# Kernel optimization log

Hardware: AMD Instinct MI355X
Metric: run time of the kernel (lower is better)

The kernel has to match this reference:

```python
import jax, jax.numpy as jnp
import numpy as np

NEG_INF = -1e30
EPS = 1e-7  # keras.backend.epsilon()


def _ctc_loss(y_true, y_pred):
    """Faithful CTC loss matching keras ctc_batch_cost + tf v1 ctc_loss.

    y_true: [B, L] int labels (no blanks), all rows full length L.
    y_pred: [B, T, C] probabilities; tf ctc_loss re-softmaxes log(p+eps).
    Blank index = C - 1. Returns loss [B, 1].
    """
    B, T, C = y_pred.shape
    L = y_true.shape[1]
    S = 2 * L + 1
    blank = C - 1

    # keras passes log(y_pred+eps) as logits; tf ctc_loss applies softmax
    lp = jax.nn.log_softmax(jnp.log(y_pred + EPS), axis=-1)  # [B,T,C]

    # extended label sequence: blank, l0, blank, l1, ..., blank  [B,S]
    ext = jnp.full((B, S), blank, dtype=y_true.dtype)
    ext = ext.at[:, 1::2].set(y_true)

    # skip transition (s-2 -> s) allowed iff ext[s] != blank and ext[s] != ext[s-2]
    same_as_2back = jnp.concatenate(
        [jnp.ones((B, 2), bool), ext[:, 2:] == ext[:, :-2]], axis=1)
    can_skip = (ext != blank) & (~same_as_2back)  # [B,S]

    # emission log-prob of each lattice state at each time: [B,T,S]
    lp_ext = jnp.take_along_axis(lp, ext[:, None, :], axis=2)

    # alpha init at t=0: only states 0 (blank) and 1 (first label) reachable
    alpha0 = jnp.full((B, S), NEG_INF, dtype=lp.dtype)
    alpha0 = alpha0.at[:, 0].set(lp_ext[:, 0, 0])
    alpha0 = alpha0.at[:, 1].set(lp_ext[:, 0, 1])

    pad1 = jnp.full((B, 1), NEG_INF, dtype=lp.dtype)
    pad2 = jnp.full((B, 2), NEG_INF, dtype=lp.dtype)

    def step(alpha, lp_t):
        a_stay = alpha
        a_prev = jnp.concatenate([pad1, alpha[:, :-1]], axis=1)
        a_skip = jnp.where(can_skip,
                           jnp.concatenate([pad2, alpha[:, :-2]], axis=1),
                           NEG_INF)
        m = jnp.maximum(a_stay, jnp.maximum(a_prev, a_skip))
        lse = m + jnp.log(jnp.exp(a_stay - m) + jnp.exp(a_prev - m)
                          + jnp.exp(a_skip - m))
        return lse + lp_t, None

    # scan over remaining T-1 time steps
    alphaT, _ = jax.lax.scan(step, alpha0, jnp.swapaxes(lp_ext, 0, 1)[1:])

    # total log-likelihood: end at last blank or last label
    loglik = jnp.logaddexp(alphaT[:, S - 1], alphaT[:, S - 2])
    return -loglik[:, None]  # [B,1], matches expand_dims(..., 1)


def setup_inputs() -> dict:
    key = jax.random.key(0)
    k1, k2 = jax.random.split(key)
    B, T, C, L = 128, 1024, 128, 128
    y_true = jax.random.randint(k1, (B, L), 0, C - 1, dtype=jnp.int32)
    y_pred = jax.random.uniform(k2, (B, T, C), dtype=jnp.float32)
    return {"y_true": y_true, "y_pred": y_pred}


def reference(y_true, y_pred):
    return _ctc_loss(y_true, y_pred)
```

## Files before the change

### kernel.cpp

```cpp
#include <hip/hip_runtime.h>

#define TT 1024
#define CC 128
#define LL 128
#define EPSF 1e-7f
#define LN2F 0.69314718055994531f

#define LOG2F(x) __builtin_amdgcn_logf(x)

typedef unsigned int uint;

template <int CTRL>
__device__ __forceinline__ int dpp_i(int old_, int x) {
  return __builtin_amdgcn_update_dpp(old_, x, CTRL, 0xf, 0xf, false);
}
template <int CTRL>
__device__ __forceinline__ float dpp0f(float x) {
  return __uint_as_float((uint)__builtin_amdgcn_update_dpp(
      0, (int)__float_as_uint(x), CTRL, 0xf, 0xf, true));
}
__device__ __forceinline__ float dpp_shr1_f32(float x) {
  return __uint_as_float((uint)__builtin_amdgcn_update_dpp(
      0, (int)__float_as_uint(x), 0x138, 0xf, 0xf, true));
}
__device__ __forceinline__ float readlane63_f(float v) {
  return __uint_as_float(
      (uint)__builtin_amdgcn_readlane((int)__float_as_uint(v), 63));
}

__device__ __forceinline__ uint bf16bits(float x) {
  uint u = __float_as_uint(x);
  return (u + 0x7fffu + ((u >> 16) & 1u)) >> 16;
}

__device__ __forceinline__ float bperm(int byteaddr, float v) {
  return __uint_as_float(
      (uint)__builtin_amdgcn_ds_bpermute(byteaddr, (int)__float_as_uint(v)));
}


#define CTC_STEP(wv, pbf)                                   \
  do {                                                      \
    const float p1 = __uint_as_float((wv) << 16);           \
    const float p2 = __uint_as_float((wv) & 0xffff0000u);   \
    const float pb = (pbf);                                 \
    const float p3 = dpp_shr1_f32(a3);                      \
    const float n0 = (a0 + p3) * pb;                        \
    const float n1 = __builtin_fmaf(s1f, p3, a0 + a1) * p1; \
    const float n2 = (a2 + a1) * pb;                        \
    const float n3 = __builtin_fmaf(s3f, a1, a3 + a2) * p2; \
    const float n4 = (a4 + a3) * pb;                        \
    a0 = n0; a1 = n1; a2 = n2; a3 = n3; a4 = n4;            \
  } while (0)

#define CTC_QUAD(et, eb)      \
  do {                        \
    CTC_STEP((et).x, (eb).x); \
    CTC_STEP((et).y, (eb).y); \
    CTC_STEP((et).z, (eb).z); \
    CTC_STEP((et).w, (eb).w); \
  } while (0)

#define CTC_RESCALE()                                                \
  do {                                                               \
    const float m = fmaxf(fmaxf(fmaxf(a0, a1), fmaxf(a2, a3)), a4);  \
    int ke = (int)(__float_as_uint(m) >> 23);                        \
    ke = max(ke, dpp_i<0x111>(ke, ke));                              \
    ke = max(ke, dpp_i<0x112>(ke, ke));                              \
    ke = max(ke, dpp_i<0x114>(ke, ke));                              \
    ke = max(ke, dpp_i<0x118>(ke, ke));                              \
    ke = max(ke, dpp_i<0x142>(ke, ke));                              \
    ke = max(ke, dpp_i<0x143>(ke, ke));                              \
    ke = __builtin_amdgcn_readlane(ke, 63);                          \
    int e = ke - 227;             \
    e = e < -127 ? -127 : e;                                         \
    const float sc = __uint_as_float((uint)(127 - e) << 23);         \
    a0 *= sc; a1 *= sc; a2 *= sc; a3 *= sc; a4 *= sc;                \
    ell += e;                                                        \
  } while (0)

#define STAGE8(t0)                                                          \
  do {                                                                      \
    float2 vv[8];                                                           \
    _Pragma("unroll") for (int j = 0; j < 8; ++j)                           \
        vv[j] = *(const float2*)(Pb + (size_t)((t0) + j) * CC);             \
    float ss[8];                                                            \
    _Pragma("unroll") for (int j = 0; j < 8; ++j)                           \
        ss[j] = (vv[j].x + vv[j].y) + (2.0f * EPSF);                        \
    _Pragma("unroll") for (int j = 0; j < 8; ++j)                           \
        ss[j] += dpp0f<0x111>(ss[j]);                        \
    _Pragma("unroll") for (int j = 0; j < 8; ++j)                           \
        ss[j] += dpp0f<0x112>(ss[j]);                        \
    _Pragma("unroll") for (int j = 0; j < 8; ++j)                           \
        ss[j] += dpp0f<0x114>(ss[j]);                        \
    _Pragma("unroll") for (int j = 0; j < 8; ++j)                           \
        ss[j] += dpp0f<0x118>(ss[j]);                        \
    _Pragma("unroll") for (int j = 0; j < 8; ++j)                           \
        ss[j] += dpp0f<0x142>(ss[j]);                      \
    _Pragma("unroll") for (int j = 0; j < 8; ++j)                           \
        ss[j] += dpp0f<0x143>(ss[j]);    \
    _Pragma("unroll") for (int q = 0; q < 2; ++q) {                         \
      uint wds[4];                                                          \
      float nys[4];                                                         \
      _Pragma("unroll") for (int c = 0; c < 4; ++c) {                       \
        const int j = q * 4 + c;                                            \
        const float x = readlane63_f(ss[j]);                                \
        const float r = 1.0f / x;                                           \
        const float er = EPSF * r;                                          \
        const float nx = __builtin_fmaf(vv[j].x, r, er);                    \
        const float ny = __builtin_fmaf(vv[j].y, r, er);                    \
        const float c1a = bperm(gxb, nx), c1b = bperm(gxb, ny);             \
        const float c2a = bperm(gyb, nx), c2b = bperm(gyb, ny);             \
        const float g1 = sx ? c1b : c1a;                                    \
        const float g2 = sy ? c2b : c2a;                                    \
        wds[c] = (bf16bits(g2) << 16) | bf16bits(g1);                       \
        nys[c] = ny;                                                        \
      }                                                                     \
      const int tq = (t0) + q * 4;                                          \
      uint4 val;                                                            \
      val.x = wds[0]; val.y = wds[1]; val.z = wds[2]; val.w = wds[3];       \
      *(uint4*)((char*)ETl + ((tq >> 5) & 3) * 8192 +                       \
                ((tq >> 2) & 7) * 1024 + L * 16) = val;                     \
      if (L == 63) {                                                        \
        float4 e4;                                                          \
        e4.x = nys[0]; e4.y = nys[1]; e4.z = nys[2]; e4.w = nys[3];         \
        *(float4*)&EBl[tq] = e4;                                            \
      }                                                                     \
    }                                                                       \
  } while (0)

__global__ __launch_bounds__(320) void ctc_fused(const int* __restrict__ yt,
                                                 const float* __restrict__ yp,
                                                 float* __restrict__ out) {
  const int b = blockIdx.x;
  const int tid = threadIdx.x;
  const int L = tid & 63;
  const int w = tid >> 6;

  __shared__ uint4 ETl[4][8][64];
  __shared__ __align__(16) float EBl[TT];

  const int2 lab = *(const int2*)(yt + b * LL + 2 * L);

  const int labm1 = __shfl_up(lab.y, 1);
  const float s1f = ((L > 0) && (lab.x != labm1)) ? 1.0f : 0.0f;
  const float s3f = (lab.y != lab.x) ? 1.0f : 0.0f;

  const float* Pb = yp + (size_t)b * TT * CC + 2 * L;
  const int gxb = (lab.x >> 1) << 2, gyb = (lab.y >> 1) << 2;
  const int sx = lab.x & 1, sy = lab.y & 1;

  if (w != 0) {
    STAGE8((w - 1) * 8);
    STAGE8(32 + (w - 1) * 8);
  }
  __syncthreads();

  uint4 etA = {0, 0, 0, 0}, etB = {0, 0, 0, 0};
  float4 ebA = {0, 0, 0, 0}, ebB = {0, 0, 0, 0};
  if (w == 0) {
    etA = ((const uint4*)ETl)[L];
    ebA = *(const float4*)&EBl[0];
  }

  float a0 = (w == 0 && L == 0) ? 0x1.0p100f : 0.0f;
  float a1 = 0.0f, a2 = 0.0f, a3 = 0.0f, a4 = 0.0f;
  int ell = -100;

#pragma unroll 1
  for (int kk = 0; kk < 32; ++kk) {
    if (w == 0) {
      const uint4* cur = (const uint4*)ETl + (size_t)(kk & 3) * 512;
      const float4* ebp = (const float4*)&EBl[kk * 32];
      etB = cur[1 * 64 + L]; ebB = ebp[1];
      CTC_QUAD(etA, ebA);
      etA = cur[2 * 64 + L]; ebA = ebp[2];
      CTC_QUAD(etB, ebB);
      etB = cur[3 * 64 + L]; ebB = ebp[3];
      CTC_QUAD(etA, ebA);
      etA = cur[4 * 64 + L]; ebA = ebp[4];
      CTC_QUAD(etB, ebB);
      CTC_RESCALE();
      etB = cur[5 * 64 + L]; ebB = ebp[5];
      CTC_QUAD(etA, ebA);
      etA = cur[6 * 64 + L]; ebA = ebp[6];
      CTC_QUAD(etB, ebB);
      etB = cur[7 * 64 + L]; ebB = ebp[7];
      CTC_QUAD(etA, ebA);
      etA = ((const uint4*)ETl)[(size_t)((kk + 1) & 3) * 512 + L];
      ebA = *(const float4*)&EBl[(kk < 31) ? (kk + 1) * 32 : 1020];
      CTC_QUAD(etB, ebB);
      CTC_RESCALE();
    } else if (kk < 30) {
      STAGE8((kk + 2) * 32 + (w - 1) * 8);
    }
    __syncthreads();
  }

  if (tid == 63) {
    float s = a3 + a4;
    if (s < 1e-37f) s = 1e-37f;
    out[b] = -LN2F * ((float)ell + LOG2F(s));
  }
}

extern "C" void kernel_launch(void* const* d_in, const int* in_sizes, int n_in,
                              void* d_out, int out_size, void* d_ws,
                              size_t ws_size, hipStream_t stream) {
  (void)d_ws; (void)ws_size; (void)n_in; (void)out_size;
  const int* yt = (const int*)d_in[0];
  const float* yp = (const float*)d_in[1];
  float* out = (float*)d_out;
  const int B = in_sizes[0] / LL;
  hipLaunchKernelGGL(ctc_fused, dim3(B), dim3(320), 0, stream, yt, yp, out);
}
```

Baseline: 144.1 us.

## Use three producer waves with packed bf16 bpermute gathers for emission staging

Cuts the block from five waves to four: three producer waves now stage 4-timestep groups in round-robin (8 groups per 32-step chunk) instead of four waves doing 8 steps each. Each gather now packs both normalized probabilities into one bf16 pair before a single ds_bpermute per label slot, halving the bpermute count, with the high or low half chosen afterward. This lowers wave count and LDS permute traffic per staged chunk. In exchange each producer wave does more work per chunk (two or three groups), which may lengthen the producer critical path relative to the single consumer wave.

```diff
diff --git a/kernel.cpp b/kernel.cpp
--- a/kernel.cpp
+++ b/kernel.cpp
@@ -31,11 +31,6 @@
 __device__ __forceinline__ uint bf16bits(float x) {
   uint u = __float_as_uint(x);
   return (u + 0x7fffu + ((u >> 16) & 1u)) >> 16;
-}
-
-__device__ __forceinline__ float bperm(int byteaddr, float v) {
-  return __uint_as_float(
-      (uint)__builtin_amdgcn_ds_bpermute(byteaddr, (int)__float_as_uint(v)));
 }
 
 
@@ -79,57 +74,64 @@
     ell += e;                                                        \
   } while (0)
 
-#define STAGE8(t0)                                                          \
+#define ST_LOAD(S, qg)                                          \
+  do {                                                          \
+    const float* Pq = Pb + (size_t)(qg) * 4 * CC + 2 * L;       \
+    vv##S##0 = *(const float2*)(Pq + 0 * CC);                   \
+    vv##S##1 = *(const float2*)(Pq + 1 * CC);                   \
+    vv##S##2 = *(const float2*)(Pq + 2 * CC);                   \
+    vv##S##3 = *(const float2*)(Pq + 3 * CC);                   \
+  } while (0)
+
+#define ST_COMP(S, qg)                                                      \
   do {                                                                      \
-    float2 vv[8];                                                           \
-    _Pragma("unroll") for (int j = 0; j < 8; ++j)                           \
-        vv[j] = *(const float2*)(Pb + (size_t)((t0) + j) * CC);             \
-    float ss[8];                                                            \
-    _Pragma("unroll") for (int j = 0; j < 8; ++j)                           \
-        ss[j] = (vv[j].x + vv[j].y) + (2.0f * EPSF);                        \
-    _Pragma("unroll") for (int j = 0; j < 8; ++j)                           \
+    const float2 vr0 = vv##S##0, vr1 = vv##S##1;                            \
+    const float2 vr2 = vv##S##2, vr3 = vv##S##3;                            \
+    const float2 vr[4] = {vr0, vr1, vr2, vr3};                              \
+    float ss[4];                                                            \
+    ss[0] = (vr0.x + vr0.y) + (2.0f * EPSF);                                \
+    ss[1] = (vr1.x + vr1.y) + (2.0f * EPSF);                                \
+    ss[2] = (vr2.x + vr2.y) + (2.0f * EPSF);                                \
+    ss[3] = (vr3.x + vr3.y) + (2.0f * EPSF);                                \
+    _Pragma("unroll") for (int j = 0; j < 4; ++j)                           \
         ss[j] += dpp0f<0x111>(ss[j]);                        \
-    _Pragma("unroll") for (int j = 0; j < 8; ++j)                           \
+    _Pragma("unroll") for (int j = 0; j < 4; ++j)                           \
         ss[j] += dpp0f<0x112>(ss[j]);                        \
-    _Pragma("unroll") for (int j = 0; j < 8; ++j)                           \
+    _Pragma("unroll") for (int j = 0; j < 4; ++j)                           \
         ss[j] += dpp0f<0x114>(ss[j]);                        \
-    _Pragma("unroll") for (int j = 0; j < 8; ++j)                           \
+    _Pragma("unroll") for (int j = 0; j < 4; ++j)                           \
         ss[j] += dpp0f<0x118>(ss[j]);                        \
-    _Pragma("unroll") for (int j = 0; j < 8; ++j)                           \
+    _Pragma("unroll") for (int j = 0; j < 4; ++j)                           \
         ss[j] += dpp0f<0x142>(ss[j]);                      \
-    _Pragma("unroll") for (int j = 0; j < 8; ++j)                           \
+    _Pragma("unroll") for (int j = 0; j < 4; ++j)                           \
         ss[j] += dpp0f<0x143>(ss[j]);    \
-    _Pragma("unroll") for (int q = 0; q < 2; ++q) {                         \
-      uint wds[4];                                                          \
-      float nys[4];                                                         \
-      _Pragma("unroll") for (int c = 0; c < 4; ++c) {                       \
-        const int j = q * 4 + c;                                            \
-        const float x = readlane63_f(ss[j]);                                \
-        const float r = 1.0f / x;                                           \
-        const float er = EPSF * r;                                          \
-        const float nx = __builtin_fmaf(vv[j].x, r, er);                    \
-        const float ny = __builtin_fmaf(vv[j].y, r, er);                    \
-        const float c1a = bperm(gxb, nx), c1b = bperm(gxb, ny);             \
-        const float c2a = bperm(gyb, nx), c2b = bperm(gyb, ny);             \
-        const float g1 = sx ? c1b : c1a;                                    \
-        const float g2 = sy ? c2b : c2a;                                    \
-        wds[c] = (bf16bits(g2) << 16) | bf16bits(g1);                       \
-        nys[c] = ny;                                                        \
-      }                                                                     \
-      const int tq = (t0) + q * 4;                                          \
-      uint4 val;                                                            \
-      val.x = wds[0]; val.y = wds[1]; val.z = wds[2]; val.w = wds[3];       \
-      *(uint4*)((char*)ETl + ((tq >> 5) & 3) * 8192 +                       \
-                ((tq >> 2) & 7) * 1024 + L * 16) = val;                     \
-      if (L == 63) {                                                        \
-        float4 e4;                                                          \
-        e4.x = nys[0]; e4.y = nys[1]; e4.z = nys[2]; e4.w = nys[3];         \
-        *(float4*)&EBl[tq] = e4;                                            \
-      }                                                                     \
+    uint wds[4];                                                            \
+    float nys[4];                                                           \
+    _Pragma("unroll") for (int j = 0; j < 4; ++j) {                         \
+      const float r = 1.0f / readlane63_f(ss[j]);                           \
+      const float er = EPSF * r;                                            \
+      const float nx = __builtin_fmaf(vr[j].x, r, er);                      \
+      const float ny = __builtin_fmaf(vr[j].y, r, er);                      \
+      const uint pk = (bf16bits(ny) << 16) | bf16bits(nx);                  \
+      const uint wx = (uint)__builtin_amdgcn_ds_bpermute(gxb, (int)pk);     \
+      const uint wy = (uint)__builtin_amdgcn_ds_bpermute(gyb, (int)pk);     \
+      const uint bx = sx ? (wx >> 16) : (wx & 0xffffu);                     \
+      const uint by = sy ? (wy >> 16) : (wy & 0xffffu);                     \
+      wds[j] = (by << 16) | bx;                                             \
+      nys[j] = ny;                                                          \
     }                                                                       \
-  } while (0)
-
-__global__ __launch_bounds__(320) void ctc_fused(const int* __restrict__ yt,
+    uint4 val;                                                              \
+    val.x = wds[0]; val.y = wds[1]; val.z = wds[2]; val.w = wds[3];         \
+    *(uint4*)((char*)ETl + (((qg) >> 3) & 3) * 8192 +                       \
+              ((qg) & 7) * 1024 + L * 16) = val;                            \
+    if (L == 63) {                                                          \
+      float4 e4;                                                            \
+      e4.x = nys[0]; e4.y = nys[1]; e4.z = nys[2]; e4.w = nys[3];           \
+      *(float4*)&EBl[(qg) * 4] = e4;                                        \
+    }                                                                       \
+  } while (0)
+
+__global__ __launch_bounds__(256) void ctc_fused(const int* __restrict__ yt,
                                                  const float* __restrict__ yp,
                                                  float* __restrict__ out) {
   const int b = blockIdx.x;
@@ -146,13 +148,19 @@
   const float s1f = ((L > 0) && (lab.x != labm1)) ? 1.0f : 0.0f;
   const float s3f = (lab.y != lab.x) ? 1.0f : 0.0f;
 
-  const float* Pb = yp + (size_t)b * TT * CC + 2 * L;
+  const float* Pb = yp + (size_t)b * TT * CC;
   const int gxb = (lab.x >> 1) << 2, gyb = (lab.y >> 1) << 2;
   const int sx = lab.x & 1, sy = lab.y & 1;
 
+  float2 vvA0, vvA1, vvA2, vvA3;
+  float2 vvB0, vvB1, vvB2, vvB3;
+  float2 vvC0, vvC1, vvC2, vvC3;
+
   if (w != 0) {
-    STAGE8((w - 1) * 8);
-    STAGE8(32 + (w - 1) * 8);
+    for (int q = w - 1; q < 16; q += 3) {
+      ST_LOAD(A, q);
+      ST_COMP(A, q);
+    }
   }
   __syncthreads();
 
@@ -192,7 +200,13 @@
       CTC_QUAD(etB, ebB);
       CTC_RESCALE();
     } else if (kk < 30) {
-      STAGE8((kk + 2) * 32 + (w - 1) * 8);
+      const int qb = (kk + 2) * 8 + (w - 1);
+      ST_LOAD(A, qb);
+      ST_LOAD(B, qb + 3);
+      if (w < 3) ST_LOAD(C, qb + 6);
+      ST_COMP(A, qb);
+      ST_COMP(B, qb + 3);
+      if (w < 3) ST_COMP(C, qb + 6);
     }
     __syncthreads();
   }
@@ -212,5 +226,5 @@
   const float* yp = (const float*)d_in[1];
   float* out = (float*)d_out;
   const int B = in_sizes[0] / LL;
-  hipLaunchKernelGGL(ctc_fused, dim3(B), dim3(320), 0, stream, yt, yp, out);
-}
+  hipLaunchKernelGGL(ctc_fused, dim3(B), dim3(256), 0, stream, yt, yp, out);
+}
```

Measured after the change: 135.3 us. -6.1%, faster.
